# Performance work log

Hardware: AMD Instinct MI355X
Metric: run time of the kernel (lower is better)

The kernel has to match this reference:

```python
import jax, jax.numpy as jnp
import numpy as np

B, L, PD, D, H, NB, NC = 32, 256, 164, 240, 16, 6, 250
DK = D // H            # 15
HID = 2 * D            # FeedForward hidden = out_dim*2 = 480
SCALE = 1.0 / float(np.sqrt(DK))
MAXLEN = 256


def _pos_embed(length, d):
    half = d // 2
    position = np.arange(length)[:, None]
    dim = np.arange(half)[None, :] / half
    angle = position * (1.0 / 1000.0 ** dim)
    return np.concatenate([np.sin(angle), np.cos(angle)], axis=-1).astype(np.float32)


def _ln(x, g, b, eps=1e-5):
    m = jnp.mean(x, axis=-1, keepdims=True)
    v = jnp.mean((x - m) ** 2, axis=-1, keepdims=True)
    return (x - m) * jax.lax.rsqrt(v + eps) * g + b


def setup_inputs() -> dict:
    key = jax.random.key(0)
    ks = iter(jax.random.split(key, 16))
    p = lambda shape: (jax.random.normal(next(ks), shape) * 0.02).astype(jnp.float32)
    z = lambda shape: jnp.zeros(shape, jnp.float32)
    o = lambda shape: jnp.ones(shape, jnp.float32)
    return {
        "x": jax.random.normal(next(ks), (B, L, PD), dtype=jnp.float32),
        "pos_embed": jnp.asarray(_pos_embed(MAXLEN, D)),
        "cls_embed": z((1, D)),
        "e_W1": p((PD, 2 * D)), "e_b1": z((2 * D,)), "e_g1": o((2 * D,)), "e_bn1": z((2 * D,)),
        "e_W2": p((2 * D, D)), "e_b2": z((D,)), "e_g2": o((D,)), "e_bn2": z((D,)),
        "ln1_g": o((NB, D)), "ln1_b": z((NB, D)),
        "Wq": p((NB, D, D)), "bq": z((NB, D)),
        "Wk": p((NB, D, D)), "bk": z((NB, D)),
        "Wv": p((NB, D, D)), "bv": z((NB, D)),
        "Wo": p((NB, D, D)), "bo": z((NB, D)),
        "ln2_g": o((NB, D)), "ln2_b": z((NB, D)),
        "W1": p((NB, D, HID)), "b1": z((NB, HID)),
        "W2": p((NB, HID, D)), "b2": z((NB, D)),
        "logit_W": p((D, NC)), "logit_b": z((NC,)),
    }


def reference(x, pos_embed, cls_embed,
              e_W1, e_b1, e_g1, e_bn1, e_W2, e_b2, e_g2, e_bn2,
              ln1_g, ln1_b, Wq, bq, Wk, bk, Wv, bv, Wo, bo,
              ln2_g, ln2_b, W1, b1, W2, b2, logit_W, logit_b):
    # padding mask: True where token is padding (all-zero features -> max == 0)
    pad = jnp.max(x, axis=2) == 0                      # [B, L]
    # XEmbed
    h = jax.nn.relu(_ln(x @ e_W1 + e_b1, e_g1, e_bn1))
    h = jax.nn.relu(_ln(h @ e_W2 + e_b2, e_g2, e_bn2))  # [B, L, D]
    h = h + pos_embed[:L][None]
    h = jnp.concatenate([jnp.broadcast_to(cls_embed[None], (B, 1, D)), h], axis=1)
    mask = jnp.concatenate([jnp.zeros((B, 1), bool), pad], axis=1)  # [B, L+1]
    Lp = L + 1
    for i in range(NB):
        # pre-norm attention (residual)
        y = _ln(h, ln1_g[i], ln1_b[i])
        q = (y @ Wq[i] + bq[i]).reshape(B, Lp, H, DK)
        k = (y @ Wk[i] + bk[i]).reshape(B, Lp, H, DK)
        v = (y @ Wv[i] + bv[i]).reshape(B, Lp, H, DK)
        scores = jnp.einsum('bqhd,bkhd->bhqk', q, k) * SCALE
        scores = jnp.where(mask[:, None, None, :], -10000.0, scores)
        attn = jax.nn.softmax(scores, axis=-1)
        o = jnp.einsum('bhqk,bkhd->bqhd', attn, v).reshape(B, Lp, D)
        h = h + (o @ Wo[i] + bo[i])
        # pre-norm FFN (residual)
        z2 = _ln(h, ln2_g[i], ln2_b[i])
        h = h + (jax.nn.relu(z2 @ W1[i] + b1[i]) @ W2[i] + b2[i])
    # masked mean pool over valid tokens (CLS always valid)
    w = (~mask).astype(h.dtype)[:, :, None]
    last = (h * w).sum(axis=1) / w.sum(axis=1)
    return last @ logit_W + logit_b                    # [B, NC]
```

## Files before the change

kernel.cpp:

```cpp
#include <hip/hip_runtime.h>
#include <math.h>

#define B_  32
#define L_  256
#define PD_ 164
#define D_  240
#define H_  16
#define NB_ 6
#define NC_ 250
#define DK_ 15
#define HID_ 480
#define LP_ 257
#define KP_ 288
#define SCALE_ 0.2581988897471611f
#define LOG2E_ 1.4426950408889634f

typedef __attribute__((ext_vector_type(8))) short bf16x8;
typedef __attribute__((ext_vector_type(8))) _Float16 f16x8;
typedef __attribute__((ext_vector_type(4))) float f32x4;

static __device__ inline unsigned short f2bf(float x) {
    unsigned u = __builtin_bit_cast(unsigned, x);
    u += 0x7FFFu + ((u >> 16) & 1u);
    return (unsigned short)(u >> 16);
}
static __device__ inline unsigned short f2h(float x) {
    _Float16 h = (_Float16)x;
    return __builtin_bit_cast(unsigned short, h);
}

static __device__ inline void gl2lds16(const void* g, void* l) {
    __builtin_amdgcn_global_load_lds(
        (const __attribute__((address_space(1))) unsigned int*)g,
        (__attribute__((address_space(3))) unsigned int*)l, 16, 0, 0);
}

__global__ void prep_misc(const float* __restrict__ x, unsigned short* __restrict__ xbf,
                          const float* __restrict__ bq, const float* __restrict__ bk,
                          const float* __restrict__ bv, float* __restrict__ b720,
                          float* __restrict__ mask) {
    int u = blockIdx.x;
    if (u < 8192) {
        const float* src = x + (size_t)u * PD_;
        unsigned short* dst = xbf + (size_t)u * 192;
        for (int k = threadIdx.x; k < 192; k += 64)
            dst[k] = f2bf(k < PD_ ? src[k] : 0.f);
    } else if (u < 8192 + NB_) {
        int i = u - 8192;
        for (int n = threadIdx.x; n < 720; n += 64) {
            float v = (n < 240) ? bq[i * 240 + n]
                    : (n < 480) ? bk[i * 240 + n - 240]
                                : bv[i * 240 + n - 480];
            b720[i * 720 + n] = v;
        }
    } else {
        int idx = (u - 8192 - NB_) * 64 + threadIdx.x;
        if (idx >= B_ * LP_) return;
        int b = idx / LP_, l = idx % LP_;
        if (l == 0) { mask[idx] = 0.f; return; }
        const float4* xr = (const float4*)(x + ((size_t)b * L_ + (l - 1)) * PD_);
        float4 m4 = xr[0];
        #pragma unroll 8
        for (int j = 1; j < 41; j++) {
            float4 v = xr[j];
            m4.x = fmaxf(m4.x, v.x); m4.y = fmaxf(m4.y, v.y);
            m4.z = fmaxf(m4.z, v.z); m4.w = fmaxf(m4.w, v.w);
        }
        float mx = fmaxf(fmaxf(m4.x, m4.y), fmaxf(m4.z, m4.w));
        mask[idx] = (mx == 0.f) ? 1.f : 0.f;
    }
}

__global__ __launch_bounds__(256)
void prep_weights(const float* __restrict__ e_W1, const float* __restrict__ e_W2,
                  const float* __restrict__ Wq, const float* __restrict__ Wk,
                  const float* __restrict__ Wv, const float* __restrict__ Wo,
                  const float* __restrict__ W1, const float* __restrict__ W2,
                  unsigned short* __restrict__ We1, unsigned short* __restrict__ We2,
                  unsigned short* __restrict__ Wqkv, unsigned short* __restrict__ WoT,
                  unsigned short* __restrict__ W1T, unsigned short* __restrict__ W2T) {
    int job = blockIdx.y;
    const float* src; unsigned short* dst; int K, N, Kpad;
    if (job == 0)      { src = e_W1; dst = We1; K = PD_; N = 480; Kpad = 192; }
    else if (job == 1) { src = e_W2; dst = We2; K = 480; N = 240; Kpad = 480; }
    else {
        int i = (job - 2) % 6, w = (job - 2) / 6;
        if (w == 0)      { src = Wq + (size_t)i*240*240; dst = Wqkv + (size_t)i*768*256;           K=240; N=240; Kpad=256; }
        else if (w == 1) { src = Wk + (size_t)i*240*240; dst = Wqkv + (size_t)i*768*256 + 240*256; K=240; N=240; Kpad=256; }
        else if (w == 2) { src = Wv + (size_t)i*240*240; dst = Wqkv + (size_t)i*768*256 + 480*256; K=240; N=240; Kpad=256; }
        else if (w == 3) { src = Wo + (size_t)i*240*240; dst = WoT + (size_t)i*256*256;            K=240; N=256; Kpad=256; }
        else if (w == 4) { src = W1 + (size_t)i*240*480; dst = W1T + (size_t)i*512*256;            K=240; N=480; Kpad=256; }
        else             { src = W2 + (size_t)i*480*240; dst = W2T + (size_t)i*256*480;            K=480; N=256; Kpad=480; }
    }
    int n0 = blockIdx.x * 64;
    if (n0 >= N) return;
    int realN = (N == 256) ? 240 : N;
    __shared__ float tile[64][65];
    const int tid = threadIdx.x;
    const int lrow = tid >> 4;
    const int lcol = (tid & 15) * 4;
    const int wn   = tid >> 2;
    const int wq   = tid & 3;
    for (int k0 = 0; k0 < Kpad; k0 += 64) {
        #pragma unroll
        for (int r4 = 0; r4 < 4; r4++) {
            int row = k0 + r4 * 16 + lrow;
            float4 v = {0.f, 0.f, 0.f, 0.f};
            if (row < K && n0 + lcol < realN)
                v = *(const float4*)(src + (size_t)row * realN + n0 + lcol);
            tile[r4 * 16 + lrow][lcol]     = v.x;
            tile[r4 * 16 + lrow][lcol + 1] = v.y;
            tile[r4 * 16 + lrow][lcol + 2] = v.z;
            tile[r4 * 16 + lrow][lcol + 3] = v.w;
        }
        __syncthreads();
        int n = n0 + wn;
        int kbase = k0 + wq * 16;
        if (n < N && kbase < Kpad) {
            unsigned short tmp[16];
            #pragma unroll
            for (int kk = 0; kk < 16; kk++)
                tmp[kk] = f2bf(tile[wq * 16 + kk][wn]);
            *(uint4*)(dst + (size_t)n * Kpad + kbase)     = *(uint4*)&tmp[0];
            *(uint4*)(dst + (size_t)n * Kpad + kbase + 8) = *(uint4*)&tmp[8];
        }
        __syncthreads();
    }
}

__global__ __launch_bounds__(256)
void gemm_mfma(const unsigned short* __restrict__ A,
               const unsigned short* __restrict__ Bt,
               const float* __restrict__ bias,
               float* __restrict__ C, unsigned short* __restrict__ Cbf,
               unsigned short* __restrict__ qp, unsigned short* __restrict__ kp,
               unsigned short* __restrict__ vp,
               int M, int N, int Kpad, int Cstride, int flags)
{
    __shared__ __align__(16) unsigned short As[2][128 * 32];
    __shared__ __align__(16) unsigned short Bs[2][64 * 32];
    const int tid = threadIdx.x;
    const int gx = gridDim.x, gy = gridDim.y;
    const int flat = blockIdx.x + gx * blockIdx.y;
    const int total = gx * gy;
    const int q8 = total >> 3, r8 = total & 7;
    const int cx = flat & 7, kx = flat >> 3;
    const int w = (cx < r8) ? (cx * (q8 + 1) + kx)
                            : (r8 * (q8 + 1) + (cx - r8) * q8 + kx);
    const int bmx = w / gy;
    const int bny = w - bmx * gy;
    const int bm = bmx * 128;
    const int bn = bny * 64;
    const int zs = gridDim.z, zi = blockIdx.z;
    const int wave = tid >> 6, lane = tid & 63;
    const int wm = (wave & 1) * 64, wn = (wave >> 1) * 32;
    const int lq = lane >> 4, lr = lane & 15;

    f32x4 acc[4][2];
    #pragma unroll
    for (int i = 0; i < 4; i++)
        #pragma unroll
        for (int j = 0; j < 2; j++) acc[i][j] = (f32x4){0.f, 0.f, 0.f, 0.f};

    const int srow = lane >> 2;
    const int schk = (lane & 3) << 3;
    const int nkt = Kpad >> 5;
    const int kt0 = (nkt * zi) / zs;
    const int kt1 = (nkt * (zi + 1)) / zs;

    const unsigned short* ga0 = A + (size_t)(bm + wave * 32 + srow) * Kpad + schk + kt0 * 32;
    const unsigned short* ga1 = A + (size_t)(bm + wave * 32 + 16 + srow) * Kpad + schk + kt0 * 32;
    const unsigned short* gb  = Bt + (size_t)(bn + wave * 16 + srow) * Kpad + schk + kt0 * 32;
    char* sa = (char*)As + wave * 2048;
    char* sb = (char*)Bs + wave * 1024;

    #define STAGE_(bu)  do {                       \
        gl2lds16(ga0, sa + (bu) * 8192);           \
        gl2lds16(ga1, sa + (bu) * 8192 + 1024);    \
        gl2lds16(gb,  sb + (bu) * 4096);           \
        ga0 += 32; ga1 += 32; gb += 32;            \
    } while (0)

    STAGE_(0);
    int cur = 0;
    for (int kt = kt0; kt < kt1; kt++) {
        if (kt + 1 < kt1) {
            STAGE_(cur ^ 1);
            asm volatile("s_waitcnt vmcnt(3)" ::: "memory");
        } else {
            asm volatile("s_waitcnt vmcnt(0)" ::: "memory");
        }
        asm volatile("s_barrier" ::: "memory");
        const unsigned short* Asc = (const unsigned short*)((const char*)As + cur * 8192);
        const unsigned short* Bsc = (const unsigned short*)((const char*)Bs + cur * 4096);
        bf16x8 af[4], bfr[2];
        #pragma unroll
        for (int i = 0; i < 4; i++)
            af[i] = *(const bf16x8*)&Asc[(wm + i * 16 + lr) * 32 + lq * 8];
        #pragma unroll
        for (int j = 0; j < 2; j++)
            bfr[j] = *(const bf16x8*)&Bsc[(wn + j * 16 + lr) * 32 + lq * 8];
        #pragma unroll
        for (int i = 0; i < 4; i++)
            #pragma unroll
            for (int j = 0; j < 2; j++)
                acc[i][j] = __builtin_amdgcn_mfma_f32_16x16x32_bf16(af[i], bfr[j], acc[i][j], 0, 0, 0);
        asm volatile("s_barrier" ::: "memory");
        cur ^= 1;
    }
    #undef STAGE_

    if (flags & 4) {
        #pragma unroll
        for (int j = 0; j < 2; j++) {
            int n = bn + wn + j * 16 + lr;
            if (n >= N) continue;
            int which = n / 240;
            int rem = n - which * 240;
            int hh = rem / 15;
            int c = rem - hh * 15;
            unsigned short* dst = (which == 0) ? qp : (which == 1) ? kp : vp;
            float bias_n = bias[n];
            float mult = (which == 0) ? (SCALE_ * LOG2E_) : 1.f;
            #pragma unroll
            for (int i = 0; i < 4; i++)
                #pragma unroll
                for (int r = 0; r < 4; r++) {
                    int m = bm + wm + i * 16 + lq * 4 + r;
                    if (m >= M) continue;
                    float s = (acc[i][j][r] + bias_n) * mult;
                    int b = m / LP_, l = m - b * LP_;
                    unsigned short bits = (which == 2) ? f2h(s) : f2bf(s);
                    dst[(((size_t)b * H_ + hh) * LP_ + l) * 16 + c] = bits;
                }
        }
    } else if (flags & 8) {
        #pragma unroll
        for (int i = 0; i < 4; i++)
            #pragma unroll
            for (int j = 0; j < 2; j++) {
                int n = bn + wn + j * 16 + lr;
                if (n >= N) continue;
                float bias_n = bias ? bias[n] : 0.f;
                #pragma unroll
                for (int r = 0; r < 4; r++) {
                    int m = bm + wm + i * 16 + lq * 4 + r;
                    if (m >= M) continue;
                    float s = acc[i][j][r] + bias_n;
                    if (flags & 1) s = fmaxf(s, 0.f);
                    Cbf[(size_t)m * Cstride + n] = f2bf(s);
                }
            }
    } else {
        #pragma unroll
        for (int i = 0; i < 4; i++)
            #pragma unroll
            for (int j = 0; j < 2; j++) {
                int n = bn + wn + j * 16 + lr;
                if (n >= N) continue;
                float bias_n = (bias && zi == 0) ? bias[n] : 0.f;
                #pragma unroll
                for (int r = 0; r < 4; r++) {
                    int m = bm + wm + i * 16 + lq * 4 + r;
                    if (m >= M) continue;
                    float s = acc[i][j][r] + bias_n;
                    if (flags & 1) s = fmaxf(s, 0.f);
                    size_t off = (size_t)m * Cstride + n;
                    if (flags & 2) {
                        if (zs > 1) atomicAdd(&C[off], s);
                        else C[off] += s;
                    } else C[off] = s;
                }
            }
    }
}

__global__ __launch_bounds__(256)
void gemm_row_ln(const unsigned short* __restrict__ A,
                 const unsigned short* __restrict__ Bt,
                 const float* __restrict__ bias,
                 float* __restrict__ h, unsigned short* __restrict__ ybf,
                 const float* __restrict__ lng, const float* __restrict__ lnb,
                 int M, int Kpad, int flags)
{
    __shared__ __align__(16) unsigned short As[2][64 * 32];
    __shared__ __align__(16) unsigned short Bs[2][256 * 32];
    const int tid = threadIdx.x;
    const int bm = blockIdx.x * 64;
    const int wave = tid >> 6, lane = tid & 63;
    const int wm = wave * 16;
    const int lq = lane >> 4, lr = lane & 15;
    const int srow = lane >> 2, schk = (lane & 3) << 3;
    const int nkt = Kpad >> 5;

    f32x4 acc[16];
    #pragma unroll
    for (int j = 0; j < 16; j++) acc[j] = (f32x4){0.f, 0.f, 0.f, 0.f};

    const unsigned short* ga0 = A + (size_t)(bm + wm + srow) * Kpad + schk;
    const unsigned short* gb0 = Bt + (size_t)(wave * 64 + srow) * Kpad + schk;
    char* sa = (char*)As + wave * 1024;
    char* sb = (char*)Bs + wave * 4096;

    #define STAGE_(bu)  do {                                      \
        gl2lds16(ga0, sa + (bu) * 4096);                          \
        gl2lds16(gb0,                   sb + (bu) * 16384);       \
        gl2lds16(gb0 + (size_t)16*Kpad, sb + (bu) * 16384 + 1024);\
        gl2lds16(gb0 + (size_t)32*Kpad, sb + (bu) * 16384 + 2048);\
        gl2lds16(gb0 + (size_t)48*Kpad, sb + (bu) * 16384 + 3072);\
        ga0 += 32; gb0 += 32;                                     \
    } while (0)

    STAGE_(0);
    int cur = 0;
    for (int kt = 0; kt < nkt; kt++) {
        if (kt + 1 < nkt) {
            STAGE_(cur ^ 1);
            asm volatile("s_waitcnt vmcnt(5)" ::: "memory");
        } else {
            asm volatile("s_waitcnt vmcnt(0)" ::: "memory");
        }
        asm volatile("s_barrier" ::: "memory");
        const unsigned short* Asc = (const unsigned short*)((const char*)As + cur * 4096);
        const unsigned short* Bsc = (const unsigned short*)((const char*)Bs + cur * 16384);
        bf16x8 af = *(const bf16x8*)&Asc[(wm + lr) * 32 + lq * 8];
        #pragma unroll
        for (int j = 0; j < 16; j++) {
            bf16x8 bf = *(const bf16x8*)&Bsc[(j * 16 + lr) * 32 + lq * 8];
            acc[j] = __builtin_amdgcn_mfma_f32_16x16x32_bf16(af, bf, acc[j], 0, 0, 0);
        }
        asm volatile("s_barrier" ::: "memory");
        cur ^= 1;
    }
    #undef STAGE_

    float biasj[15], gj[15], bj[15];
    #pragma unroll
    for (int j = 0; j < 15; j++) {
        int n = j * 16 + lr;
        biasj[j] = bias[n];
        if (flags & 1) { gj[j] = lng[n]; bj[j] = lnb[n]; }
    }
    #pragma unroll
    for (int r = 0; r < 4; r++) {
        const int row = bm + wm + lq * 4 + r;
        if (row >= M) continue;
        float v[15];
        float s = 0.f;
        #pragma unroll
        for (int j = 0; j < 15; j++) {
            v[j] = acc[j][r] + biasj[j] + h[(size_t)row * 240 + j * 16 + lr];
            s += v[j];
        }
        s += __shfl_xor(s, 1); s += __shfl_xor(s, 2);
        s += __shfl_xor(s, 4); s += __shfl_xor(s, 8);
        #pragma unroll
        for (int j = 0; j < 15; j++)
            h[(size_t)row * 240 + j * 16 + lr] = v[j];
        if (flags & 1) {
            const float mean = s * (1.f / 240.f);
            float q = 0.f;
            #pragma unroll
            for (int j = 0; j < 15; j++) { float d = v[j] - mean; q += d * d; }
            q += __shfl_xor(q, 1); q += __shfl_xor(q, 2);
            q += __shfl_xor(q, 4); q += __shfl_xor(q, 8);
            const float rs = rsqrtf(q * (1.f / 240.f) + 1e-5f);
            #pragma unroll
            for (int j = 0; j < 15; j++)
                ybf[(size_t)row * 256 + j * 16 + lr] =
                    f2bf((v[j] - mean) * rs * gj[j] + bj[j]);
            ybf[(size_t)row * 256 + 240 + lr] = 0;
        }
    }
}

__global__ __launch_bounds__(256)
void ln480(const float* __restrict__ in, unsigned short* __restrict__ out,
           const float* __restrict__ g, const float* __restrict__ bb) {
    const int row = blockIdx.x * 4 + (threadIdx.x >> 6);
    const int lane = threadIdx.x & 63;
    const float* x = in + (size_t)row * 480;
    float4 va = {0.f,0.f,0.f,0.f}, vb = {0.f,0.f,0.f,0.f};
    if (lane < 60) {
        va = *(const float4*)(x + lane * 8);
        vb = *(const float4*)(x + lane * 8 + 4);
    }
    float s = ((va.x + va.y) + (va.z + va.w)) + ((vb.x + vb.y) + (vb.z + vb.w));
    #pragma unroll
    for (int off = 32; off; off >>= 1) s += __shfl_xor(s, off);
    const float mean = s * (1.f / 480.f);
    float4 da, db;
    da.x = va.x - mean; da.y = va.y - mean; da.z = va.z - mean; da.w = va.w - mean;
    db.x = vb.x - mean; db.y = vb.y - mean; db.z = vb.z - mean; db.w = vb.w - mean;
    float vs = (lane < 60) ? ((da.x*da.x + da.y*da.y) + (da.z*da.z + da.w*da.w)) +
                             ((db.x*db.x + db.y*db.y) + (db.z*db.z + db.w*db.w)) : 0.f;
    #pragma unroll
    for (int off = 32; off; off >>= 1) vs += __shfl_xor(vs, off);
    const float rs = rsqrtf(vs * (1.f / 480.f) + 1e-5f);
    if (lane < 60) {
        float4 ga = *(const float4*)(g + lane * 8);
        float4 gb = *(const float4*)(g + lane * 8 + 4);
        float4 ba = *(const float4*)(bb + lane * 8);
        float4 b2 = *(const float4*)(bb + lane * 8 + 4);
        ushort4 oa, ob;
        oa.x = f2bf(fmaxf(da.x * rs * ga.x + ba.x, 0.f));
        oa.y = f2bf(fmaxf(da.y * rs * ga.y + ba.y, 0.f));
        oa.z = f2bf(fmaxf(da.z * rs * ga.z + ba.z, 0.f));
        oa.w = f2bf(fmaxf(da.w * rs * ga.w + ba.w, 0.f));
        ob.x = f2bf(fmaxf(db.x * rs * gb.x + b2.x, 0.f));
        ob.y = f2bf(fmaxf(db.y * rs * gb.y + b2.y, 0.f));
        ob.z = f2bf(fmaxf(db.z * rs * gb.z + b2.z, 0.f));
        ob.w = f2bf(fmaxf(db.w * rs * gb.w + b2.w, 0.f));
        *(ushort4*)(out + (size_t)row * 480 + lane * 8) = oa;
        *(ushort4*)(out + (size_t)row * 480 + lane * 8 + 4) = ob;
    }
}

__global__ __launch_bounds__(256)
void embed_finish(const float* __restrict__ tmp, const float* __restrict__ mask,
                  const float* __restrict__ g, const float* __restrict__ bb,
                  const float* __restrict__ pos, const float* __restrict__ cls,
                  const float* __restrict__ l1g, const float* __restrict__ l1b,
                  float* __restrict__ h, unsigned short* __restrict__ ybf,
                  unsigned short* __restrict__ qp, unsigned short* __restrict__ kp,
                  unsigned short* __restrict__ vp) {
    const int row = blockIdx.x * 4 + (threadIdx.x >> 6);
    const int lane = threadIdx.x & 63;
    const int b = row / LP_, l = row - b * LP_;
    float* outr = h + (size_t)row * 240;

    if (lane >= 60 && lane <= 62) {
        unsigned short bits;
        unsigned short* dst;
        if (lane == 60) { bits = f2bf(LOG2E_); dst = qp; }
        else if (lane == 61) { bits = (mask[row] != 0.f) ? f2bf(-10000.f) : 0; dst = kp; }
        else { bits = f2h(1.f); dst = vp; }
        #pragma unroll
        for (int hh = 0; hh < H_; hh++)
            dst[(((size_t)b * H_ + hh) * LP_ + l) * 16 + 15] = bits;
    }

    float4 o = {0.f, 0.f, 0.f, 0.f};
    if (l == 0) {
        if (lane < 60) o = *(const float4*)(cls + lane * 4);
    } else {
        const float* x = tmp + ((size_t)b * L_ + (l - 1)) * 240;
        float4 v = {0.f, 0.f, 0.f, 0.f};
        if (lane < 60) v = *(const float4*)(x + lane * 4);
        float s = (v.x + v.y) + (v.z + v.w);
        #pragma unroll
        for (int off = 32; off; off >>= 1) s += __shfl_xor(s, off);
        const float mean = s * (1.f / 240.f);
        float4 d;
        d.x = v.x - mean; d.y = v.y - mean; d.z = v.z - mean; d.w = v.w - mean;
        float vs = (lane < 60) ? (d.x * d.x + d.y * d.y) + (d.z * d.z + d.w * d.w) : 0.f;
        #pragma unroll
        for (int off = 32; off; off >>= 1) vs += __shfl_xor(vs, off);
        const float rs = rsqrtf(vs * (1.f / 240.f) + 1e-5f);
        if (lane < 60) {
            float4 g4 = *(const float4*)(g + lane * 4);
            float4 b4 = *(const float4*)(bb + lane * 4);
            float4 p4 = *(const float4*)(pos + (size_t)(l - 1) * 240 + lane * 4);
            o.x = fmaxf(d.x * rs * g4.x + b4.x, 0.f) + p4.x;
            o.y = fmaxf(d.y * rs * g4.y + b4.y, 0.f) + p4.y;
            o.z = fmaxf(d.z * rs * g4.z + b4.z, 0.f) + p4.z;
            o.w = fmaxf(d.w * rs * g4.w + b4.w, 0.f) + p4.w;
        }
    }
    if (lane < 60) *(float4*)(outr + lane * 4) = o;

    float s1 = (o.x + o.y) + (o.z + o.w);
    #pragma unroll
    for (int off = 32; off; off >>= 1) s1 += __shfl_xor(s1, off);
    const float mean1 = s1 * (1.f / 240.f);
    float4 d1;
    d1.x = o.x - mean1; d1.y = o.y - mean1; d1.z = o.z - mean1; d1.w = o.w - mean1;
    float vs1 = (lane < 60) ? (d1.x * d1.x + d1.y * d1.y) + (d1.z * d1.z + d1.w * d1.w) : 0.f;
    #pragma unroll
    for (int off = 32; off; off >>= 1) vs1 += __shfl_xor(vs1, off);
    const float rs1 = rsqrtf(vs1 * (1.f / 240.f) + 1e-5f);
    ushort4 o4 = {0, 0, 0, 0};
    if (lane < 60) {
        float4 g4 = *(const float4*)(l1g + lane * 4);
        float4 b4 = *(const float4*)(l1b + lane * 4);
        o4.x = f2bf(d1.x * rs1 * g4.x + b4.x);
        o4.y = f2bf(d1.y * rs1 * g4.y + b4.y);
        o4.z = f2bf(d1.z * rs1 * g4.z + b4.z);
        o4.w = f2bf(d1.w * rs1 * g4.w + b4.w);
    }
    *(ushort4*)(ybf + (size_t)row * 256 + lane * 4) = o4;
}

__global__ __launch_bounds__(256)
void attn_mfma(const unsigned short* __restrict__ qp, const unsigned short* __restrict__ kp,
               const unsigned short* __restrict__ vp, unsigned short* __restrict__ obf)
{
    __shared__ __align__(16) unsigned short Kl[KP_ * 24];
    __shared__ __align__(16) unsigned short Vt[16 * 296];
    __shared__ __align__(16) unsigned short Pl[4][16 * 296];
    const int hh = blockIdx.x, b = blockIdx.y;
    const int tid = threadIdx.x;
    const int wave = tid >> 6, lane = tid & 63;
    const int lq = lane >> 4, lr = lane & 15;
    const size_t base = ((size_t)b * H_ + hh) * LP_ * 16;

    for (int key = tid; key < KP_; key += 256) {
        uint4 z = {0u, 0u, 0u, 0u};
        uint4 k0 = z, k1 = z, v0 = z, v1 = z;
        if (key < LP_) {
            k0 = *(const uint4*)(kp + base + (size_t)key * 16);
            k1 = *(const uint4*)(kp + base + (size_t)key * 16 + 8);
            v0 = *(const uint4*)(vp + base + (size_t)key * 16);
            v1 = *(const uint4*)(vp + base + (size_t)key * 16 + 8);
        } else {
            k1.w = 0xC61C0000u;
        }
        *(uint4*)&Kl[key * 24] = k0;
        *(uint4*)&Kl[key * 24 + 8] = k1;
        unsigned short vs[8];
        *(uint4*)vs = v0;
        #pragma unroll
        for (int d = 0; d < 8; d++) Vt[d * 296 + key] = vs[d];
        *(uint4*)vs = v1;
        #pragma unroll
        for (int d = 0; d < 8; d++) Vt[(d + 8) * 296 + key] = vs[d];
    }
    __syncthreads();

    unsigned short* Pw = &Pl[wave][0];
    {
        int r = lane >> 2, c0 = 272 + (lane & 3) * 4;
        ushort4 z4 = {0, 0, 0, 0};
        *(ushort4*)&Pw[r * 296 + c0] = z4;
    }
    for (int qt = wave; qt < 17; qt += 4) {
        const int qrow = qt * 16 + lr;
        bf16x8 aq = {0, 0, 0, 0, 0, 0, 0, 0};
        if (lq < 2)
            aq = *(const bf16x8*)(qp + base + (size_t)qrow * 16 + lq * 8);
        for (int kt = 0; kt < 17; kt++) {
            bf16x8 bk = {0, 0, 0, 0, 0, 0, 0, 0};
            if (lq < 2)
                bk = *(const bf16x8*)&Kl[(kt * 16 + lr) * 24 + lq * 8];
            f32x4 sacc = {0.f, 0.f, 0.f, 0.f};
            sacc = __builtin_amdgcn_mfma_f32_16x16x32_bf16(aq, bk, sacc, 0, 0, 0);
            #pragma unroll
            for (int r = 0; r < 4; r++)
                Pw[(lq * 4 + r) * 296 + kt * 16 + lr] = f2h(exp2f(sacc[r]));
        }
        asm volatile("s_waitcnt lgkmcnt(0)" ::: "memory");
        f32x4 o = {0.f, 0.f, 0.f, 0.f};
        __builtin_amdgcn_s_setprio(1);
        #pragma unroll
        for (int ks = 0; ks < 9; ks++) {
            f16x8 ap = *(const f16x8*)&Pw[lr * 296 + ks * 32 + lq * 8];
            f16x8 bv = *(const f16x8*)&Vt[lr * 296 + ks * 32 + lq * 8];
            o = __builtin_amdgcn_mfma_f32_16x16x32_f16(ap, bv, o, 0, 0, 0);
        }
        __builtin_amdgcn_s_setprio(0);
        asm volatile("s_waitcnt lgkmcnt(0)" ::: "memory");
        #pragma unroll
        for (int r = 0; r < 4; r++) {
            float denom = __shfl(o[r], lane | 15);
            int q = qt * 16 + lq * 4 + r;
            if (q < LP_ && lr < 15)
                obf[((size_t)b * LP_ + q) * 256 + hh * DK_ + lr] = f2bf(o[r] / denom);
        }
    }
    if (hh == 0) {
        for (int q = tid; q < LP_; q += 256) {
            uint4 z = {0u, 0u, 0u, 0u};
            *(uint4*)(obf + ((size_t)b * LP_ + q) * 256 + 240) = z;
            *(uint4*)(obf + ((size_t)b * LP_ + q) * 256 + 248) = z;
        }
    }
}

__global__ void pool_partial(const float* __restrict__ h, const float* __restrict__ mask,
                             float* __restrict__ partial) {
    int b = blockIdx.x, slice = blockIdx.y;
    int d = threadIdx.x;
    if (d >= D_) return;
    float s = 0.f;
    int l0 = slice * 29;
    for (int i = 0; i < 29; i++) {
        int l = l0 + i;
        if (l < LP_ && mask[b * LP_ + l] == 0.f)
            s += h[((size_t)b * LP_ + l) * D_ + d];
    }
    partial[((size_t)b * 9 + slice) * D_ + d] = s;
}

__global__ __launch_bounds__(256)
void pool_logits(const float* __restrict__ partial, const float* __restrict__ mask,
                 const float* __restrict__ W, const float* __restrict__ bias,
                 float* __restrict__ out) {
    int b = blockIdx.x;
    int t = threadIdx.x;
    __shared__ float red[256];
    __shared__ float pool[240];
    float c = 0.f;
    for (int l = t; l < LP_; l += 256) c += (mask[b * LP_ + l] == 0.f) ? 1.f : 0.f;
    red[t] = c;
    __syncthreads();
    for (int off = 128; off > 0; off >>= 1) {
        if (t < off) red[t] += red[t + off];
        __syncthreads();
    }
    float inv = 1.f / red[0];
    if (t < D_) {
        float s = 0.f;
        #pragma unroll
        for (int sl = 0; sl < 9; sl++) s += partial[((size_t)b * 9 + sl) * D_ + t];
        pool[t] = s * inv;
    }
    __syncthreads();
    if (t < NC_) {
        float s = bias[t];
        for (int kk = 0; kk < D_; kk++) s += pool[kk] * W[(size_t)kk * NC_ + t];
        out[b * NC_ + t] = s;
    }
}

extern "C" void kernel_launch(void* const* d_in, const int* in_sizes, int n_in,
                              void* d_out, int out_size, void* d_ws, size_t ws_size,
                              hipStream_t stream) {
    const float* x        = (const float*)d_in[0];
    const float* pos      = (const float*)d_in[1];
    const float* cls      = (const float*)d_in[2];
    const float* e_W1     = (const float*)d_in[3];
    const float* e_b1     = (const float*)d_in[4];
    const float* e_g1     = (const float*)d_in[5];
    const float* e_bn1    = (const float*)d_in[6];
    const float* e_W2     = (const float*)d_in[7];
    const float* e_b2     = (const float*)d_in[8];
    const float* e_g2     = (const float*)d_in[9];
    const float* e_bn2    = (const float*)d_in[10];
    const float* ln1_g    = (const float*)d_in[11];
    const float* ln1_b    = (const float*)d_in[12];
    const float* Wq       = (const float*)d_in[13];
    const float* bq       = (const float*)d_in[14];
    const float* Wk       = (const float*)d_in[15];
    const float* bk       = (const float*)d_in[16];
    const float* Wv       = (const float*)d_in[17];
    const float* bv       = (const float*)d_in[18];
    const float* Wo       = (const float*)d_in[19];
    const float* bo       = (const float*)d_in[20];
    const float* ln2_g    = (const float*)d_in[21];
    const float* ln2_b    = (const float*)d_in[22];
    const float* W1       = (const float*)d_in[23];
    const float* b1       = (const float*)d_in[24];
    const float* W2       = (const float*)d_in[25];
    const float* b2       = (const float*)d_in[26];
    const float* logit_W  = (const float*)d_in[27];
    const float* logit_b  = (const float*)d_in[28];
    float* out = (float*)d_out;

    const size_t TOK  = (size_t)B_ * LP_;
    const size_t TOKP = 8320;
    const size_t HN   = TOK * D_;
    const size_t QN   = (size_t)B_ * H_ * LP_ * 16;

    char* wsb = (char*)d_ws;
    size_t cur = 0;
    auto take = [&](size_t bytes) { void* p = wsb + cur; cur += (bytes + 15) & ~15ULL; return p; };
    float* mask = (float*)take(8224 * 4);
    float* h    = (float*)take(HN * 4);
    float* b720 = (float*)take(NB_ * 720 * 4);
    float* part = (float*)take((size_t)B_ * 9 * D_ * 4);
    void* regionA = take((size_t)8192 * 480 * 4);
    float* tmp1 = (float*)regionA;
    unsigned short* tbf = (unsigned short*)regionA;
    void* regionB = take(TOKP * 256 * 2 * 2);
    float* y32 = (float*)regionB;
    unsigned short* ybf = (unsigned short*)regionB;
    unsigned short* obf = ybf + TOKP * 256;
    unsigned short* xbf  = (unsigned short*)take((size_t)8192 * 192 * 2);
    unsigned short* We1  = (unsigned short*)take((size_t)512 * 192 * 2);
    unsigned short* We2  = (unsigned short*)take((size_t)256 * 480 * 2);
    unsigned short* Wqkv = (unsigned short*)take((size_t)NB_ * 768 * 256 * 2);
    unsigned short* WoT  = (unsigned short*)take((size_t)NB_ * 256 * 256 * 2);
    unsigned short* W1T  = (unsigned short*)take((size_t)NB_ * 512 * 256 * 2);
    unsigned short* W2T  = (unsigned short*)take((size_t)NB_ * 256 * 480 * 2);
    unsigned short* qp = (unsigned short*)take(QN * 3 * 2 + 16 * 16 * 2);
    unsigned short* kp = qp + QN;
    unsigned short* vp = kp + QN;
    unsigned short* t480bf = qp;

    const int BS = 256;

    prep_misc<<<8192 + NB_ + 129, 64, 0, stream>>>(x, xbf, bq, bk, bv, b720, mask);
    prep_weights<<<dim3(8, 38), BS, 0, stream>>>(e_W1, e_W2, Wq, Wk, Wv, Wo, W1, W2,
                                                 We1, We2, Wqkv, WoT, W1T, W2T);

    gemm_mfma<<<dim3(64, 8), BS, 0, stream>>>(xbf, We1, e_b1, tmp1, nullptr,
                                              nullptr, nullptr, nullptr,
                                              8192, 480, 192, 480, 0);
    ln480<<<2048, BS, 0, stream>>>(tmp1, t480bf, e_g1, e_bn1);
    gemm_mfma<<<dim3(64, 4), BS, 0, stream>>>(t480bf, We2, e_b2, y32, nullptr,
                                              nullptr, nullptr, nullptr,
                                              8192, 240, 480, 240, 0);
    embed_finish<<<(int)(TOK / 4), BS, 0, stream>>>(y32, mask, e_g2, e_bn2, pos, cls,
                                                    ln1_g, ln1_b, h, ybf, qp, kp, vp);

    for (int i = 0; i < NB_; i++) {
        gemm_mfma<<<dim3(65, 12), BS, 0, stream>>>(ybf, Wqkv + (size_t)i * 768 * 256,
                                                   b720 + i * 720, nullptr, nullptr,
                                                   qp, kp, vp,
                                                   (int)TOK, 720, 256, 0, 4);
        attn_mfma<<<dim3(H_, B_), BS, 0, stream>>>(qp, kp, vp, obf);
        gemm_row_ln<<<129, BS, 0, stream>>>(obf, WoT + (size_t)i * 256 * 256,
                                            bo + i * D_, h, ybf,
                                            ln2_g + i * D_, ln2_b + i * D_,
                                            (int)TOK, 256, 1);
        gemm_mfma<<<dim3(65, 8), BS, 0, stream>>>(ybf, W1T + (size_t)i * 512 * 256,
                                                  b1 + i * HID_, nullptr, tbf,
                                                  nullptr, nullptr, nullptr,
                                                  (int)TOK, 480, 256, 480, 1 | 8);
        gemm_row_ln<<<129, BS, 0, stream>>>(tbf, W2T + (size_t)i * 256 * 480,
                                            b2 + i * D_, h, ybf,
                                            ln1_g + ((i + 1) % NB_) * D_,
                                            ln1_b + ((i + 1) % NB_) * D_,
                                            (int)TOK, 480, (i < NB_ - 1) ? 1 : 0);
    }

    pool_partial<<<dim3(B_, 9), BS, 0, stream>>>(h, mask, part);
    pool_logits<<<B_, BS, 0, stream>>>(part, mask, logit_W, logit_b, out);
}
```

Measured before the change: 708.0 us.

## Fuse FFN up-projection, ReLU and down-projection with residual LayerNorm into one kernel

Replaces the separate W1 GEMM and the W2 GEMM-plus-LayerNorm launches with a single kernel per layer. Each block handles 32 token rows and keeps the ReLU'd 480-wide hidden activation in LDS as bf16, so it is never written to or read back from global memory. The second GEMM then adds bias and residual and applies the next layer's LayerNorm. In exchange there is one block per CU with large LDS use and no double buffering. Only half the waves issue MFMAs in the second GEMM, and every block reloads the full W1 and W2 weights.

After: 703.7 us. No clear change (-0.6%).

```diff
diff --git a/kernel.cpp b/kernel.cpp
--- a/kernel.cpp
+++ b/kernel.cpp
@@ -350,6 +350,129 @@
         #pragma unroll
         for (int j = 0; j < 15; j++) {
             v[j] = acc[j][r] + biasj[j] + h[(size_t)row * 240 + j * 16 + lr];
+            s += v[j];
+        }
+        s += __shfl_xor(s, 1); s += __shfl_xor(s, 2);
+        s += __shfl_xor(s, 4); s += __shfl_xor(s, 8);
+        #pragma unroll
+        for (int j = 0; j < 15; j++)
+            h[(size_t)row * 240 + j * 16 + lr] = v[j];
+        if (flags & 1) {
+            const float mean = s * (1.f / 240.f);
+            float q = 0.f;
+            #pragma unroll
+            for (int j = 0; j < 15; j++) { float d = v[j] - mean; q += d * d; }
+            q += __shfl_xor(q, 1); q += __shfl_xor(q, 2);
+            q += __shfl_xor(q, 4); q += __shfl_xor(q, 8);
+            const float rs = rsqrtf(q * (1.f / 240.f) + 1e-5f);
+            #pragma unroll
+            for (int j = 0; j < 15; j++)
+                ybf[(size_t)row * 256 + j * 16 + lr] =
+                    f2bf((v[j] - mean) * rs * gj[j] + bj[j]);
+            ybf[(size_t)row * 256 + 240 + lr] = 0;
+        }
+    }
+}
+
+__global__ __launch_bounds__(256)
+void ffn_fused(const unsigned short* __restrict__ ybf_in,
+               const unsigned short* __restrict__ W1t,
+               const float* __restrict__ b1,
+               const unsigned short* __restrict__ W2t,
+               const float* __restrict__ b2,
+               float* __restrict__ h, unsigned short* __restrict__ ybf,
+               const float* __restrict__ lng, const float* __restrict__ lnb,
+               int flags)
+{
+    __shared__ __align__(16) unsigned short Tl[32 * 488];
+    __shared__ __align__(16) unsigned short St[17408];
+    unsigned short* Al = St;
+    unsigned short* B1 = St + 1024;
+    unsigned short* B2 = St;
+    const int tid = threadIdx.x;
+    const int bm = blockIdx.x * 32;
+    const int wave = tid >> 6, lane = tid & 63;
+    const int rg = wave >> 1, ch = wave & 1;
+    const int lq = lane >> 4, lr = lane & 15;
+    const int srow = lane >> 2, schk = (lane & 3) << 3;
+
+    f32x4 acc1[15];
+    #pragma unroll
+    for (int j = 0; j < 15; j++) acc1[j] = (f32x4){0.f, 0.f, 0.f, 0.f};
+
+    const unsigned short* gaA = ybf_in + (size_t)(bm + wave * 16 + srow) * 256 + schk;
+    const unsigned short* gb1 = W1t + (size_t)(wave * 128 + srow) * 256 + schk;
+
+    for (int kt = 0; kt < 8; kt++) {
+        if (wave < 2)
+            gl2lds16(gaA, (char*)Al + wave * 1024);
+        #pragma unroll
+        for (int s = 0; s < 8; s++)
+            gl2lds16(gb1 + (size_t)s * 16 * 256, (char*)B1 + (wave * 8 + s) * 1024);
+        gaA += 32; gb1 += 32;
+        asm volatile("s_waitcnt vmcnt(0)" ::: "memory");
+        asm volatile("s_barrier" ::: "memory");
+        bf16x8 af = *(const bf16x8*)&Al[(rg * 16 + lr) * 32 + lq * 8];
+        #pragma unroll
+        for (int j = 0; j < 15; j++) {
+            bf16x8 bf = *(const bf16x8*)&B1[(ch * 240 + j * 16 + lr) * 32 + lq * 8];
+            acc1[j] = __builtin_amdgcn_mfma_f32_16x16x32_bf16(af, bf, acc1[j], 0, 0, 0);
+        }
+        asm volatile("s_barrier" ::: "memory");
+    }
+
+    #pragma unroll
+    for (int j = 0; j < 15; j++) {
+        const int col = ch * 240 + j * 16 + lr;
+        const float bb = b1[col];
+        #pragma unroll
+        for (int r = 0; r < 4; r++) {
+            const int row = rg * 16 + lq * 4 + r;
+            Tl[row * 488 + col] = f2bf(fmaxf(acc1[j][r] + bb, 0.f));
+        }
+    }
+    __syncthreads();
+
+    f32x4 acc2[15];
+    #pragma unroll
+    for (int j = 0; j < 15; j++) acc2[j] = (f32x4){0.f, 0.f, 0.f, 0.f};
+
+    const unsigned short* gb2 = W2t + (size_t)(wave * 64 + srow) * 480 + schk;
+
+    for (int kt = 0; kt < 15; kt++) {
+        #pragma unroll
+        for (int s = 0; s < 4; s++)
+            gl2lds16(gb2 + (size_t)s * 16 * 480, (char*)B2 + (wave * 4 + s) * 1024);
+        gb2 += 32;
+        asm volatile("s_waitcnt vmcnt(0)" ::: "memory");
+        asm volatile("s_barrier" ::: "memory");
+        if (wave < 2) {
+            bf16x8 af = *(const bf16x8*)&Tl[(wave * 16 + lr) * 488 + kt * 32 + lq * 8];
+            #pragma unroll
+            for (int j = 0; j < 15; j++) {
+                bf16x8 bf = *(const bf16x8*)&B2[(j * 16 + lr) * 32 + lq * 8];
+                acc2[j] = __builtin_amdgcn_mfma_f32_16x16x32_bf16(af, bf, acc2[j], 0, 0, 0);
+            }
+        }
+        asm volatile("s_barrier" ::: "memory");
+    }
+
+    if (wave >= 2) return;
+    float biasj[15], gj[15], bj[15];
+    #pragma unroll
+    for (int j = 0; j < 15; j++) {
+        int n = j * 16 + lr;
+        biasj[j] = b2[n];
+        if (flags & 1) { gj[j] = lng[n]; bj[j] = lnb[n]; }
+    }
+    #pragma unroll
+    for (int r = 0; r < 4; r++) {
+        const int row = bm + wave * 16 + lq * 4 + r;
+        float v[15];
+        float s = 0.f;
+        #pragma unroll
+        for (int j = 0; j < 15; j++) {
+            v[j] = acc2[j][r] + biasj[j] + h[(size_t)row * 240 + j * 16 + lr];
             s += v[j];
         }
         s += __shfl_xor(s, 1); s += __shfl_xor(s, 2);
@@ -713,15 +836,13 @@
                                             bo + i * D_, h, ybf,
                                             ln2_g + i * D_, ln2_b + i * D_,
                                             (int)TOK, 256, 1);
-        gemm_mfma<<<dim3(65, 8), BS, 0, stream>>>(ybf, W1T + (size_t)i * 512 * 256,
-                                                  b1 + i * HID_, nullptr, tbf,
-                                                  nullptr, nullptr, nullptr,
-                                                  (int)TOK, 480, 256, 480, 1 | 8);
-        gemm_row_ln<<<129, BS, 0, stream>>>(tbf, W2T + (size_t)i * 256 * 480,
-                                            b2 + i * D_, h, ybf,
-                                            ln1_g + ((i + 1) % NB_) * D_,
-                                            ln1_b + ((i + 1) % NB_) * D_,
-                                            (int)TOK, 480, (i < NB_ - 1) ? 1 : 0);
+        ffn_fused<<<257, BS, 0, stream>>>(ybf, W1T + (size_t)i * 512 * 256,
+                                          b1 + i * HID_,
+                                          W2T + (size_t)i * 256 * 480,
+                                          b2 + i * D_, h, ybf,
+                                          ln1_g + ((i + 1) % NB_) * D_,
+                                          ln1_b + ((i + 1) % NB_) * D_,
+                                          (i < NB_ - 1) ? 1 : 0);
     }
 
     pool_partial<<<dim3(B_, 9), BS, 0, stream>>>(h, mask, part);
```
